# Kernel optimization log

Measured on AMD Instinct MI355X. Metric: run time of the kernel, lower is better.

Reference implementation:

```python
import jax, jax.numpy as jnp
import numpy as np

N_NODES = 100000
N_EDGES = 800000
F_IN, N_HID, N_CLS = 256, 128, 40


def setup_inputs() -> dict:
    key = jax.random.key(0)
    ks = jax.random.split(key, 6)
    features = jax.random.normal(ks[0], (N_NODES, F_IN), dtype=jnp.float32)
    src = jax.random.randint(ks[1], (N_EDGES,), 0, N_NODES, dtype=jnp.int64)
    dst = jax.random.randint(ks[2], (N_EDGES,), 0, N_NODES, dtype=jnp.int64)
    W1 = jax.random.normal(ks[3], (F_IN, N_HID), dtype=jnp.float32) / np.sqrt(F_IN)
    b1 = jnp.zeros((N_HID,), dtype=jnp.float32)
    W2 = jax.random.normal(ks[4], (N_HID, N_CLS), dtype=jnp.float32) / np.sqrt(N_HID)
    b2 = jnp.zeros((N_CLS,), dtype=jnp.float32)
    return {"features": features, "src": src, "dst": dst,
            "W1": W1, "b1": b1, "W2": W2, "b2": b2}


def reference(features, src, dst, W1, b1, W2, b2):
    # DGL GraphConv with norm='both': h = D_dst^{-1/2} A (D_src^{-1/2} x) W + b
    # Eval mode: dropout(p=0.85) is identity.
    N = features.shape[0]
    ones = jnp.ones(src.shape[0], dtype=features.dtype)
    out_deg = jax.ops.segment_sum(ones, src, num_segments=N)
    in_deg = jax.ops.segment_sum(ones, dst, num_segments=N)
    norm_src = jnp.where(out_deg > 0, out_deg ** -0.5, 0.0)[:, None]  # [N,1]
    norm_dst = jnp.where(in_deg > 0, in_deg ** -0.5, 0.0)[:, None]

    def gconv(x, W, b):
        # project first (in_feats >= out_feats here) to shrink SpMM width
        h = (x * norm_src) @ W                                # [N, out]
        agg = jax.ops.segment_sum(h[src], dst, num_segments=N)  # sparse aggregate
        return agg * norm_dst + b

    x = jax.nn.relu(gconv(features, W1, b1))
    return gconv(x, W2, b2)
```

## Files before the change

### kernel.cpp

```cpp
#include <hip/hip_runtime.h>
#include <hip/hip_bf16.h>
#include <math.h>


#define F_IN  256
#define F_HID 128
#define F_CLS 40

#define RSZ 8192
#define NSL 32

typedef __bf16 bf16_t;
typedef bf16_t bf16x8 __attribute__((ext_vector_type(8)));
typedef float floatx4 __attribute__((ext_vector_type(4)));

static __device__ __forceinline__ unsigned short f2b(float f) {
    __hip_bfloat16 h = __float2bfloat16(f);
    return __builtin_bit_cast(unsigned short, h);
}
static __device__ __forceinline__ float b2f(unsigned short u) {
    return __uint_as_float((unsigned)u << 16);
}

__global__ __launch_bounds__(256) void hist_kernel(
    const int* __restrict__ src, const int* __restrict__ dst,
    unsigned* __restrict__ partial_s, unsigned* __restrict__ partial_d, int E)
{
    __shared__ unsigned h[RSZ];
    const int t = threadIdx.x;
    const int r  = blockIdx.x / NSL;
    const int sl = blockIdx.x % NSL;
    const int lo = r * RSZ;
    const int* __restrict__ keys = blockIdx.y ? dst : src;
    unsigned* __restrict__ part = blockIdx.y ? partial_d : partial_s;

    for (int i = t; i < RSZ; i += 256) h[i] = 0;
    __syncthreads();

    const int slice = (E + NSL - 1) / NSL;
    const int e0 = sl * slice;
    const int e1 = min(E, e0 + slice);

    int e = e0 + t;
    for (; e + 7 * 256 < e1; e += 8 * 256) {
        int k[8];
        #pragma unroll
        for (int i = 0; i < 8; ++i) k[i] = keys[e + i * 256];
        #pragma unroll
        for (int i = 0; i < 8; ++i) {
            unsigned kk = (unsigned)(k[i] - lo);
            if (kk < RSZ) atomicAdd(&h[kk], 1u);
        }
    }
    for (; e < e1; e += 256) {
        unsigned kk = (unsigned)(keys[e] - lo);
        if (kk < RSZ) atomicAdd(&h[kk], 1u);
    }
    __syncthreads();

    unsigned* dst_p = part + (size_t)blockIdx.x * RSZ;
    for (int i = t; i < RSZ; i += 256) dst_p[i] = h[i];
}

__global__ __launch_bounds__(256) void degnorm_kernel(
    const unsigned* __restrict__ partial_s, const unsigned* __restrict__ partial_d,
    int* __restrict__ cnt_dst, float* __restrict__ norm_src,
    float* __restrict__ norm_dst, int N)
{
    int i = blockIdx.x * 256 + threadIdx.x;
    if (i >= N) return;
    int r = i / RSZ;
    int off = i & (RSZ - 1);
    const unsigned* ps = partial_s + (size_t)r * NSL * RSZ + off;
    const unsigned* pd = partial_d + (size_t)r * NSL * RSZ + off;
    unsigned ss = 0, sd = 0;
    #pragma unroll
    for (int sl = 0; sl < NSL; ++sl) {
        ss += ps[(size_t)sl * RSZ];
        sd += pd[(size_t)sl * RSZ];
    }
    cnt_dst[i] = (int)sd;
    norm_src[i] = ss ? 1.0f / sqrtf((float)ss) : 0.0f;
    norm_dst[i] = sd ? 1.0f / sqrtf((float)sd) : 0.0f;
}

__global__ __launch_bounds__(256) void scan1_kernel(const int* __restrict__ cnt,
                                                    int* __restrict__ row_off,
                                                    int* __restrict__ blk_sums, int N) {
    __shared__ int s[256];
    const int t = threadIdx.x;
    const int base = blockIdx.x * 1024 + t * 4;
    int v0 = (base + 0 < N) ? cnt[base + 0] : 0;
    int v1 = (base + 1 < N) ? cnt[base + 1] : 0;
    int v2 = (base + 2 < N) ? cnt[base + 2] : 0;
    int v3 = (base + 3 < N) ? cnt[base + 3] : 0;
    int local = v0 + v1 + v2 + v3;
    s[t] = local;
    __syncthreads();
    for (int off = 1; off < 256; off <<= 1) {
        int x = (t >= off) ? s[t - off] : 0;
        __syncthreads();
        s[t] += x;
        __syncthreads();
    }
    int excl = s[t] - local;
    if (t == 255) blk_sums[blockIdx.x] = s[t];
    if (base + 0 < N) row_off[base + 0] = excl;
    if (base + 1 < N) row_off[base + 1] = excl + v0;
    if (base + 2 < N) row_off[base + 2] = excl + v0 + v1;
    if (base + 3 < N) row_off[base + 3] = excl + v0 + v1 + v2;
}

__global__ __launch_bounds__(256) void scan2_kernel(int* __restrict__ blk_sums, int B) {
    __shared__ int s[256];
    const int t = threadIdx.x;
    int local = (t < B) ? blk_sums[t] : 0;
    s[t] = local;
    __syncthreads();
    for (int off = 1; off < 256; off <<= 1) {
        int x = (t >= off) ? s[t - off] : 0;
        __syncthreads();
        s[t] += x;
        __syncthreads();
    }
    if (t < B) blk_sums[t] = s[t] - local;
}

__global__ __launch_bounds__(256) void scan3_kernel(int* __restrict__ row_off,
                                                    const int* __restrict__ blk_sums,
                                                    int N, int E) {
    const int t = threadIdx.x;
    const int base = blockIdx.x * 1024 + t * 4;
    const int add = blk_sums[blockIdx.x];
    #pragma unroll
    for (int i = 0; i < 4; ++i) {
        int idx = base + i;
        if (idx < N) row_off[idx] += add;
    }
    if (blockIdx.x == 0 && t == 0) row_off[N] = E;
}

__global__ __launch_bounds__(256) void slicepref_kernel(
    unsigned* __restrict__ partial_d, const int* __restrict__ row_off,
    int N, int NRtot)
{
    int idx = blockIdx.x * 256 + threadIdx.x;
    if (idx >= NRtot) return;
    int r = idx / RSZ;
    int i = idx & (RSZ - 1);
    unsigned run = (idx < N) ? (unsigned)row_off[idx] : 0u;
    unsigned* p = partial_d + (size_t)r * NSL * RSZ + i;
    #pragma unroll
    for (int sl = 0; sl < NSL; ++sl) {
        unsigned c = p[(size_t)sl * RSZ];
        p[(size_t)sl * RSZ] = run;
        run += c;
    }
}

__global__ __launch_bounds__(256) void scatter2_kernel(
    const int* __restrict__ src, const int* __restrict__ dst,
    const unsigned* __restrict__ pref, int* __restrict__ csr_src, int E)
{
    __shared__ unsigned cur[RSZ];
    const int t = threadIdx.x;
    const int r  = blockIdx.x / NSL;
    const int sl = blockIdx.x % NSL;
    const int lo = r * RSZ;
    const unsigned* p = pref + (size_t)blockIdx.x * RSZ;

    for (int i = t; i < RSZ; i += 256) cur[i] = p[i];
    __syncthreads();

    const int slice = (E + NSL - 1) / NSL;
    const int e0 = sl * slice;
    const int e1 = min(E, e0 + slice);

    int e = e0 + t;
    for (; e + 7 * 256 < e1; e += 8 * 256) {
        int d[8], s[8];
        #pragma unroll
        for (int i = 0; i < 8; ++i) { d[i] = dst[e + i * 256]; s[i] = src[e + i * 256]; }
        #pragma unroll
        for (int i = 0; i < 8; ++i) {
            unsigned k = (unsigned)(d[i] - lo);
            if (k < RSZ) {
                unsigned pos = atomicAdd(&cur[k], 1u);
                csr_src[pos] = s[i];
            }
        }
    }
    for (; e < e1; e += 256) {
        unsigned k = (unsigned)(dst[e] - lo);
        if (k < RSZ) {
            unsigned pos = atomicAdd(&cur[k], 1u);
            csr_src[pos] = src[e];
        }
    }
}

__global__ __launch_bounds__(256) void pack_w1t_kernel(const float* __restrict__ W1,
                                                       __hip_bfloat16* __restrict__ W1t) {
    int idx = blockIdx.x * 256 + threadIdx.x;
    int n = idx >> 8;
    int k = idx & 255;
    W1t[idx] = __float2bfloat16(W1[(size_t)k * F_HID + n]);
}

__global__ __launch_bounds__(256, 4) void gemm1_mfma_kernel(
    const float* __restrict__ X, const __hip_bfloat16* __restrict__ W1t,
    const float* __restrict__ norm_src, __hip_bfloat16* __restrict__ h1b, int N)
{
    __shared__ __hip_bfloat16 Bs[2][128][72];
    const int t = threadIdx.x;
    const int node0 = blockIdx.x * 64;
    const int lane = t & 63;
    const int w = t >> 6;
    const int l15 = lane & 15;
    const int quad = lane >> 4;

    const int arow = node0 + w * 16 + l15;
    const bool valid = arow < N;
    const int arow_c = valid ? arow : (N - 1);
    const float ns = valid ? norm_src[arow] : 0.0f;

    const int bn = t >> 1;
    const int bh = t & 1;
    const __hip_bfloat16* wp = W1t + (size_t)bn * F_IN + bh * 32;
    const float* xp = X + (size_t)arow_c * F_IN + quad * 8;

    uint4  breg[4];
    float4 araw[4];

    #pragma unroll
    for (int i = 0; i < 4; ++i) breg[i] = *(const uint4*)(wp + i * 8);
    araw[0] = *(const float4*)(xp + 0);
    araw[1] = *(const float4*)(xp + 4);
    araw[2] = *(const float4*)(xp + 32);
    araw[3] = *(const float4*)(xp + 36);

    floatx4 acc[8] = {};

    #pragma unroll
    for (int c = 0; c < 4; ++c) {
        #pragma unroll
        for (int j = 0; j < 4; ++j)
            *(uint4*)&Bs[c & 1][bn][bh * 32 + j * 8] = breg[j];
        __syncthreads();
        bf16x8 ab0, ab1;
        {
            union { bf16x8 v; unsigned short u[8]; } cv;
            cv.u[0] = f2b(araw[0].x * ns); cv.u[1] = f2b(araw[0].y * ns);
            cv.u[2] = f2b(araw[0].z * ns); cv.u[3] = f2b(araw[0].w * ns);
            cv.u[4] = f2b(araw[1].x * ns); cv.u[5] = f2b(araw[1].y * ns);
            cv.u[6] = f2b(araw[1].z * ns); cv.u[7] = f2b(araw[1].w * ns);
            ab0 = cv.v;
            cv.u[0] = f2b(araw[2].x * ns); cv.u[1] = f2b(araw[2].y * ns);
            cv.u[2] = f2b(araw[2].z * ns); cv.u[3] = f2b(araw[2].w * ns);
            cv.u[4] = f2b(araw[3].x * ns); cv.u[5] = f2b(araw[3].y * ns);
            cv.u[6] = f2b(araw[3].z * ns); cv.u[7] = f2b(araw[3].w * ns);
            ab1 = cv.v;
        }
        if (c < 3) {
            #pragma unroll
            for (int i = 0; i < 4; ++i)
                breg[i] = *(const uint4*)(wp + (c + 1) * 64 + i * 8);
            araw[0] = *(const float4*)(xp + (c + 1) * 64 + 0);
            araw[1] = *(const float4*)(xp + (c + 1) * 64 + 4);
            araw[2] = *(const float4*)(xp + (c + 1) * 64 + 32);
            araw[3] = *(const float4*)(xp + (c + 1) * 64 + 36);
        }
        #pragma unroll
        for (int nt = 0; nt < 8; ++nt) {
            bf16x8 b = *(const bf16x8*)&Bs[c & 1][nt * 16 + l15][quad * 8];
            acc[nt] = __builtin_amdgcn_mfma_f32_16x16x32_bf16(ab0, b, acc[nt], 0, 0, 0);
        }
        #pragma unroll
        for (int nt = 0; nt < 8; ++nt) {
            bf16x8 b = *(const bf16x8*)&Bs[c & 1][nt * 16 + l15][32 + quad * 8];
            acc[nt] = __builtin_amdgcn_mfma_f32_16x16x32_bf16(ab1, b, acc[nt], 0, 0, 0);
        }
    }

    #pragma unroll
    for (int nt = 0; nt < 8; ++nt) {
        #pragma unroll
        for (int r = 0; r < 4; ++r) {
            int node = node0 + w * 16 + quad * 4 + r;
            if (node < N)
                h1b[(size_t)node * F_HID + nt * 16 + l15] = __float2bfloat16(acc[nt][r]);
        }
    }
}

__global__ __launch_bounds__(320) void spmm_gemm2_kernel(
    const __hip_bfloat16* __restrict__ h1b, const int* __restrict__ row_off,
    const int* __restrict__ csr_src, const float* __restrict__ W2,
    const float* __restrict__ b1, const float* __restrict__ norm_src,
    const float* __restrict__ norm_dst, float* __restrict__ h2, int N)
{
    __shared__ float As[64][132];
    __shared__ float Ws[128][40];
    const int t = threadIdx.x;
    const int node0 = blockIdx.x * 64;

    #pragma unroll
    for (int i = 0; i < 4; ++i) {
        int f = t + 320 * i;
        int r = f / 10;
        int kk = (f % 10) * 4;
        *(float4*)&Ws[r][kk] = *(const float4*)(W2 + (size_t)r * F_CLS + kk);
    }

    const int g = t >> 4;
    const int cc = (t & 15) << 3;
    for (int n = g; n < 64; n += 20) {
        int node = node0 + n;
        float4 a0 = make_float4(0.f, 0.f, 0.f, 0.f);
        float4 a1 = make_float4(0.f, 0.f, 0.f, 0.f);
        if (node < N) {
            const int start = row_off[node];
            const int end = row_off[node + 1];
            int j = start;
            for (; j + 4 <= end; j += 4) {
                int s0 = csr_src[j + 0];
                int s1 = csr_src[j + 1];
                int s2 = csr_src[j + 2];
                int s3 = csr_src[j + 3];
                union { uint4 v; unsigned short u[8]; } q0, q1, q2, q3;
                q0.v = *(const uint4*)(h1b + (size_t)s0 * F_HID + cc);
                q1.v = *(const uint4*)(h1b + (size_t)s1 * F_HID + cc);
                q2.v = *(const uint4*)(h1b + (size_t)s2 * F_HID + cc);
                q3.v = *(const uint4*)(h1b + (size_t)s3 * F_HID + cc);
                a0.x += b2f(q0.u[0]) + b2f(q1.u[0]) + b2f(q2.u[0]) + b2f(q3.u[0]);
                a0.y += b2f(q0.u[1]) + b2f(q1.u[1]) + b2f(q2.u[1]) + b2f(q3.u[1]);
                a0.z += b2f(q0.u[2]) + b2f(q1.u[2]) + b2f(q2.u[2]) + b2f(q3.u[2]);
                a0.w += b2f(q0.u[3]) + b2f(q1.u[3]) + b2f(q2.u[3]) + b2f(q3.u[3]);
                a1.x += b2f(q0.u[4]) + b2f(q1.u[4]) + b2f(q2.u[4]) + b2f(q3.u[4]);
                a1.y += b2f(q0.u[5]) + b2f(q1.u[5]) + b2f(q2.u[5]) + b2f(q3.u[5]);
                a1.z += b2f(q0.u[6]) + b2f(q1.u[6]) + b2f(q2.u[6]) + b2f(q3.u[6]);
                a1.w += b2f(q0.u[7]) + b2f(q1.u[7]) + b2f(q2.u[7]) + b2f(q3.u[7]);
            }
            for (; j < end; ++j) {
                int s = csr_src[j];
                union { uint4 v; unsigned short u[8]; } q;
                q.v = *(const uint4*)(h1b + (size_t)s * F_HID + cc);
                a0.x += b2f(q.u[0]); a0.y += b2f(q.u[1]);
                a0.z += b2f(q.u[2]); a0.w += b2f(q.u[3]);
                a1.x += b2f(q.u[4]); a1.y += b2f(q.u[5]);
                a1.z += b2f(q.u[6]); a1.w += b2f(q.u[7]);
            }
            float nd = norm_dst[node];
            float ns2 = norm_src[node];
            float4 bb0 = *(const float4*)(b1 + cc);
            float4 bb1 = *(const float4*)(b1 + cc + 4);
            a0.x = fmaxf(fmaf(a0.x, nd, bb0.x), 0.f) * ns2;
            a0.y = fmaxf(fmaf(a0.y, nd, bb0.y), 0.f) * ns2;
            a0.z = fmaxf(fmaf(a0.z, nd, bb0.z), 0.f) * ns2;
            a0.w = fmaxf(fmaf(a0.w, nd, bb0.w), 0.f) * ns2;
            a1.x = fmaxf(fmaf(a1.x, nd, bb1.x), 0.f) * ns2;
            a1.y = fmaxf(fmaf(a1.y, nd, bb1.y), 0.f) * ns2;
            a1.z = fmaxf(fmaf(a1.z, nd, bb1.z), 0.f) * ns2;
            a1.w = fmaxf(fmaf(a1.w, nd, bb1.w), 0.f) * ns2;
        }
        *(float4*)&As[n][cc] = a0;
        *(float4*)&As[n][cc + 4] = a1;
    }
    __syncthreads();

    const int col = t % 40;
    const int rowg = t / 40;
    float acc[8] = {};
    #pragma unroll 8
    for (int k = 0; k < F_HID; ++k) {
        float w = Ws[k][col];
        #pragma unroll
        for (int i = 0; i < 8; ++i)
            acc[i] = fmaf(As[rowg * 8 + i][k], w, acc[i]);
    }
    #pragma unroll
    for (int i = 0; i < 8; ++i) {
        int node = node0 + rowg * 8 + i;
        if (node < N) h2[(size_t)node * F_CLS + col] = acc[i];
    }
}

__global__ __launch_bounds__(256) void spmm2_csr_kernel(
    const float* __restrict__ h2, const int* __restrict__ row_off,
    const int* __restrict__ csr_src, const float* __restrict__ norm_dst,
    const float* __restrict__ b2, float* __restrict__ out, int N)
{
    const int t = threadIdx.x;
    const int node = blockIdx.x * 16 + (t >> 4);
    const int lane = t & 15;
    if (node >= N || lane >= 10) return;
    const int c = lane << 2;
    const int start = row_off[node];
    const int end = row_off[node + 1];
    float4 acc = make_float4(0.f, 0.f, 0.f, 0.f);
    int j = start;
    for (; j + 4 <= end; j += 4) {
        int s0 = csr_src[j + 0];
        int s1 = csr_src[j + 1];
        int s2 = csr_src[j + 2];
        int s3 = csr_src[j + 3];
        float4 v0 = *(const float4*)(h2 + (size_t)s0 * F_CLS + c);
        float4 v1 = *(const float4*)(h2 + (size_t)s1 * F_CLS + c);
        float4 v2 = *(const float4*)(h2 + (size_t)s2 * F_CLS + c);
        float4 v3 = *(const float4*)(h2 + (size_t)s3 * F_CLS + c);
        acc.x += v0.x + v1.x + v2.x + v3.x;
        acc.y += v0.y + v1.y + v2.y + v3.y;
        acc.z += v0.z + v1.z + v2.z + v3.z;
        acc.w += v0.w + v1.w + v2.w + v3.w;
    }
    for (; j < end; ++j) {
        int s = csr_src[j];
        float4 v = *(const float4*)(h2 + (size_t)s * F_CLS + c);
        acc.x += v.x; acc.y += v.y; acc.z += v.z; acc.w += v.w;
    }
    float nd = norm_dst[node];
    float4 bb = *(const float4*)(b2 + c);
    float4 r;
    r.x = fmaf(acc.x, nd, bb.x);
    r.y = fmaf(acc.y, nd, bb.y);
    r.z = fmaf(acc.z, nd, bb.z);
    r.w = fmaf(acc.w, nd, bb.w);
    *(float4*)(out + (size_t)node * F_CLS + c) = r;
}

extern "C" void kernel_launch(void* const* d_in, const int* in_sizes, int n_in,
                              void* d_out, int out_size, void* d_ws, size_t ws_size,
                              hipStream_t stream) {
    const float* X   = (const float*)d_in[0];
    const int*   src = (const int*)d_in[1];
    const int*   dst = (const int*)d_in[2];
    const float* W1  = (const float*)d_in[3];
    const float* b1  = (const float*)d_in[4];
    const float* W2  = (const float*)d_in[5];
    const float* b2  = (const float*)d_in[6];
    float* out = (float*)d_out;

    const int N = in_sizes[0] / F_IN;
    const int E = in_sizes[1];
    const int NB = (N + 1023) / 1024;
    const int NR = (N + RSZ - 1) / RSZ;
    const int NRtot = NR * RSZ;

    char* w = (char*)d_ws;
    int*   cnt_dst  = (int*)w;                      w += (size_t)N * 4;
    int*   row_off  = (int*)w;                      w += (size_t)(N + 4) * 4;
    int*   blk_sums = (int*)w;                      w += 256 * 4;
    int*   csr_src  = (int*)w;                      w += (size_t)E * 4;
    float* norm_src = (float*)w;                    w += (size_t)N * 4;
    float* norm_dst = (float*)w;                    w += (size_t)N * 4;
    float* h2       = (float*)w;                    w += (size_t)N * F_CLS * 4;
    __hip_bfloat16* W1t = (__hip_bfloat16*)w;       w += (size_t)F_HID * F_IN * 2;
    __hip_bfloat16* h1b = (__hip_bfloat16*)w;       w += (size_t)N * F_HID * 2;
    unsigned* partial_s = (unsigned*)w;             w += (size_t)NR * NSL * RSZ * 4;
    unsigned* partial_d = (unsigned*)w;             w += (size_t)NR * NSL * RSZ * 4;

    hist_kernel<<<dim3(NR * NSL, 2), 256, 0, stream>>>(src, dst, partial_s, partial_d, E);
    degnorm_kernel<<<(N + 255) / 256, 256, 0, stream>>>(partial_s, partial_d,
                                                        cnt_dst, norm_src, norm_dst, N);

    scan1_kernel<<<NB, 256, 0, stream>>>(cnt_dst, row_off, blk_sums, N);
    scan2_kernel<<<1, 256, 0, stream>>>(blk_sums, NB);
    scan3_kernel<<<NB, 256, 0, stream>>>(row_off, blk_sums, N, E);

    slicepref_kernel<<<(NRtot + 255) / 256, 256, 0, stream>>>(partial_d, row_off, N, NRtot);
    scatter2_kernel<<<NR * NSL, 256, 0, stream>>>(src, dst, partial_d, csr_src, E);

    pack_w1t_kernel<<<(F_HID * F_IN) / 256, 256, 0, stream>>>(W1, W1t);

    gemm1_mfma_kernel<<<(N + 63) / 64, 256, 0, stream>>>(X, W1t, norm_src, h1b, N);

    spmm_gemm2_kernel<<<(N + 63) / 64, 320, 0, stream>>>(h1b, row_off, csr_src, W2,
                                                         b1, norm_src, norm_dst, h2, N);

    spmm2_csr_kernel<<<(N + 15) / 16, 256, 0, stream>>>(h2, row_off, csr_src, norm_dst, b2, out, N);
}
```

Baseline: 373.5 us.

## Split fused SpMM+GEMM2 into separate CSR gather kernel and GEMM2 kernel

The fused layer-1 aggregation plus second projection kernel is split in two. A standalone SpMM kernel assigns one 32-lane group per node, gathers bf16 rows with 8-way unrolled loads and writes an fp32 agg1 buffer. A separate GEMM2 kernel then reads agg1, applies bias, ReLU and norms, and multiplies by W2. The split is meant to give the irregular gather more parallelism and memory-level concurrency, at the cost of an extra N×128 fp32 round trip through global memory and one more launch; the layer-2 SpMM gather loop is also unrolled to 8.

```diff
diff --git a/kernel.cpp b/kernel.cpp
--- a/kernel.cpp
+++ b/kernel.cpp
@@ -293,9 +293,57 @@
     }
 }
 
-__global__ __launch_bounds__(320) void spmm_gemm2_kernel(
+__global__ __launch_bounds__(256) void spmm1_csr_kernel(
     const __hip_bfloat16* __restrict__ h1b, const int* __restrict__ row_off,
-    const int* __restrict__ csr_src, const float* __restrict__ W2,
+    const int* __restrict__ csr_src, float* __restrict__ agg1, int N)
+{
+    const int t = threadIdx.x;
+    const int node = blockIdx.x * 8 + (t >> 5);
+    if (node >= N) return;
+    const int c = (t & 31) << 2;
+    const int start = row_off[node];
+    const int end = row_off[node + 1];
+    float4 acc = make_float4(0.f, 0.f, 0.f, 0.f);
+    int j = start;
+    for (; j + 8 <= end; j += 8) {
+        int s[8];
+        #pragma unroll
+        for (int i = 0; i < 8; ++i) s[i] = csr_src[j + i];
+        ushort4 u[8];
+        #pragma unroll
+        for (int i = 0; i < 8; ++i)
+            u[i] = *(const ushort4*)(h1b + (size_t)s[i] * F_HID + c);
+        #pragma unroll
+        for (int i = 0; i < 8; ++i) {
+            acc.x += b2f(u[i].x);
+            acc.y += b2f(u[i].y);
+            acc.z += b2f(u[i].z);
+            acc.w += b2f(u[i].w);
+        }
+    }
+    for (; j + 2 <= end; j += 2) {
+        int s0 = csr_src[j + 0];
+        int s1 = csr_src[j + 1];
+        ushort4 u0 = *(const ushort4*)(h1b + (size_t)s0 * F_HID + c);
+        ushort4 u1 = *(const ushort4*)(h1b + (size_t)s1 * F_HID + c);
+        acc.x += b2f(u0.x) + b2f(u1.x);
+        acc.y += b2f(u0.y) + b2f(u1.y);
+        acc.z += b2f(u0.z) + b2f(u1.z);
+        acc.w += b2f(u0.w) + b2f(u1.w);
+    }
+    if (j < end) {
+        int s = csr_src[j];
+        ushort4 u = *(const ushort4*)(h1b + (size_t)s * F_HID + c);
+        acc.x += b2f(u.x);
+        acc.y += b2f(u.y);
+        acc.z += b2f(u.z);
+        acc.w += b2f(u.w);
+    }
+    *(float4*)(agg1 + (size_t)node * F_HID + c) = acc;
+}
+
+__global__ __launch_bounds__(320) void gemm2_kernel(
+    const float* __restrict__ agg1, const float* __restrict__ W2,
     const float* __restrict__ b1, const float* __restrict__ norm_src,
     const float* __restrict__ norm_dst, float* __restrict__ h2, int N)
 {
@@ -311,60 +359,22 @@
         int kk = (f % 10) * 4;
         *(float4*)&Ws[r][kk] = *(const float4*)(W2 + (size_t)r * F_CLS + kk);
     }
-
-    const int g = t >> 4;
-    const int cc = (t & 15) << 3;
-    for (int n = g; n < 64; n += 20) {
-        int node = node0 + n;
-        float4 a0 = make_float4(0.f, 0.f, 0.f, 0.f);
-        float4 a1 = make_float4(0.f, 0.f, 0.f, 0.f);
+    for (int f = t; f < 2048; f += 320) {
+        int r = f >> 5;
+        int kk = (f & 31) << 2;
+        int node = node0 + r;
+        float4 v = make_float4(0.f, 0.f, 0.f, 0.f);
         if (node < N) {
-            const int start = row_off[node];
-            const int end = row_off[node + 1];
-            int j = start;
-            for (; j + 4 <= end; j += 4) {
-                int s0 = csr_src[j + 0];
-                int s1 = csr_src[j + 1];
-                int s2 = csr_src[j + 2];
-                int s3 = csr_src[j + 3];
-                union { uint4 v; unsigned short u[8]; } q0, q1, q2, q3;
-                q0.v = *(const uint4*)(h1b + (size_t)s0 * F_HID + cc);
-                q1.v = *(const uint4*)(h1b + (size_t)s1 * F_HID + cc);
-                q2.v = *(const uint4*)(h1b + (size_t)s2 * F_HID + cc);
-                q3.v = *(const uint4*)(h1b + (size_t)s3 * F_HID + cc);
-                a0.x += b2f(q0.u[0]) + b2f(q1.u[0]) + b2f(q2.u[0]) + b2f(q3.u[0]);
-                a0.y += b2f(q0.u[1]) + b2f(q1.u[1]) + b2f(q2.u[1]) + b2f(q3.u[1]);
-                a0.z += b2f(q0.u[2]) + b2f(q1.u[2]) + b2f(q2.u[2]) + b2f(q3.u[2]);
-                a0.w += b2f(q0.u[3]) + b2f(q1.u[3]) + b2f(q2.u[3]) + b2f(q3.u[3]);
-                a1.x += b2f(q0.u[4]) + b2f(q1.u[4]) + b2f(q2.u[4]) + b2f(q3.u[4]);
-                a1.y += b2f(q0.u[5]) + b2f(q1.u[5]) + b2f(q2.u[5]) + b2f(q3.u[5]);
-                a1.z += b2f(q0.u[6]) + b2f(q1.u[6]) + b2f(q2.u[6]) + b2f(q3.u[6]);
-                a1.w += b2f(q0.u[7]) + b2f(q1.u[7]) + b2f(q2.u[7]) + b2f(q3.u[7]);
-            }
-            for (; j < end; ++j) {
-                int s = csr_src[j];
-                union { uint4 v; unsigned short u[8]; } q;
-                q.v = *(const uint4*)(h1b + (size_t)s * F_HID + cc);
-                a0.x += b2f(q.u[0]); a0.y += b2f(q.u[1]);
-                a0.z += b2f(q.u[2]); a0.w += b2f(q.u[3]);
-                a1.x += b2f(q.u[4]); a1.y += b2f(q.u[5]);
-                a1.z += b2f(q.u[6]); a1.w += b2f(q.u[7]);
-            }
+            float4 a = *(const float4*)(agg1 + (size_t)node * F_HID + kk);
             float nd = norm_dst[node];
-            float ns2 = norm_src[node];
-            float4 bb0 = *(const float4*)(b1 + cc);
-            float4 bb1 = *(const float4*)(b1 + cc + 4);
-            a0.x = fmaxf(fmaf(a0.x, nd, bb0.x), 0.f) * ns2;
-            a0.y = fmaxf(fmaf(a0.y, nd, bb0.y), 0.f) * ns2;
-            a0.z = fmaxf(fmaf(a0.z, nd, bb0.z), 0.f) * ns2;
-            a0.w = fmaxf(fmaf(a0.w, nd, bb0.w), 0.f) * ns2;
-            a1.x = fmaxf(fmaf(a1.x, nd, bb1.x), 0.f) * ns2;
-            a1.y = fmaxf(fmaf(a1.y, nd, bb1.y), 0.f) * ns2;
-            a1.z = fmaxf(fmaf(a1.z, nd, bb1.z), 0.f) * ns2;
-            a1.w = fmaxf(fmaf(a1.w, nd, bb1.w), 0.f) * ns2;
-        }
-        *(float4*)&As[n][cc] = a0;
-        *(float4*)&As[n][cc + 4] = a1;
+            float ns = norm_src[node];
+            float4 bb = *(const float4*)(b1 + kk);
+            v.x = fmaxf(fmaf(a.x, nd, bb.x), 0.f) * ns;
+            v.y = fmaxf(fmaf(a.y, nd, bb.y), 0.f) * ns;
+            v.z = fmaxf(fmaf(a.z, nd, bb.z), 0.f) * ns;
+            v.w = fmaxf(fmaf(a.w, nd, bb.w), 0.f) * ns;
+        }
+        *(float4*)&As[r][kk] = v;
     }
     __syncthreads();
 
@@ -399,21 +409,30 @@
     const int end = row_off[node + 1];
     float4 acc = make_float4(0.f, 0.f, 0.f, 0.f);
     int j = start;
-    for (; j + 4 <= end; j += 4) {
+    for (; j + 8 <= end; j += 8) {
+        int s[8];
+        #pragma unroll
+        for (int i = 0; i < 8; ++i) s[i] = csr_src[j + i];
+        float4 v[8];
+        #pragma unroll
+        for (int i = 0; i < 8; ++i)
+            v[i] = *(const float4*)(h2 + (size_t)s[i] * F_CLS + c);
+        #pragma unroll
+        for (int i = 0; i < 8; ++i) {
+            acc.x += v[i].x; acc.y += v[i].y; acc.z += v[i].z; acc.w += v[i].w;
+        }
+    }
+    for (; j + 2 <= end; j += 2) {
         int s0 = csr_src[j + 0];
         int s1 = csr_src[j + 1];
-        int s2 = csr_src[j + 2];
-        int s3 = csr_src[j + 3];
         float4 v0 = *(const float4*)(h2 + (size_t)s0 * F_CLS + c);
         float4 v1 = *(const float4*)(h2 + (size_t)s1 * F_CLS + c);
-        float4 v2 = *(const float4*)(h2 + (size_t)s2 * F_CLS + c);
-        float4 v3 = *(const float4*)(h2 + (size_t)s3 * F_CLS + c);
-        acc.x += v0.x + v1.x + v2.x + v3.x;
-        acc.y += v0.y + v1.y + v2.y + v3.y;
-        acc.z += v0.z + v1.z + v2.z + v3.z;
-        acc.w += v0.w + v1.w + v2.w + v3.w;
-    }
-    for (; j < end; ++j) {
+        acc.x += v0.x + v1.x;
+        acc.y += v0.y + v1.y;
+        acc.z += v0.z + v1.z;
+        acc.w += v0.w + v1.w;
+    }
+    if (j < end) {
         int s = csr_src[j];
         float4 v = *(const float4*)(h2 + (size_t)s * F_CLS + c);
         acc.x += v.x; acc.y += v.y; acc.z += v.z; acc.w += v.w;
@@ -453,6 +472,7 @@
     int*   csr_src  = (int*)w;                      w += (size_t)E * 4;
     float* norm_src = (float*)w;                    w += (size_t)N * 4;
     float* norm_dst = (float*)w;                    w += (size_t)N * 4;
+    float* agg1     = (float*)w;                    w += (size_t)N * F_HID * 4;
     float* h2       = (float*)w;                    w += (size_t)N * F_CLS * 4;
     __hip_bfloat16* W1t = (__hip_bfloat16*)w;       w += (size_t)F_HID * F_IN * 2;
     __hip_bfloat16* h1b = (__hip_bfloat16*)w;       w += (size_t)N * F_HID * 2;
@@ -474,8 +494,9 @@
 
     gemm1_mfma_kernel<<<(N + 63) / 64, 256, 0, stream>>>(X, W1t, norm_src, h1b, N);
 
-    spmm_gemm2_kernel<<<(N + 63) / 64, 320, 0, stream>>>(h1b, row_off, csr_src, W2,
-                                                         b1, norm_src, norm_dst, h2, N);
+    spmm1_csr_kernel<<<(N + 7) / 8, 256, 0, stream>>>(h1b, row_off, csr_src, agg1, N);
+
+    gemm2_kernel<<<(N + 63) / 64, 320, 0, stream>>>(agg1, W2, b1, norm_src, norm_dst, h2, N);
 
     spmm2_csr_kernel<<<(N + 15) / 16, 256, 0, stream>>>(h2, row_off, csr_src, norm_dst, b2, out, N);
 }
```

Result: faster. 364.4 us (-2.4%).
